# Kernel tuning notes

Measured on AMD Instinct MI355X. Metric: run time of the kernel, lower is better.

The kernel has to match this reference:

```python
import jax, jax.numpy as jnp
import numpy as np

D_EMB = 1024
D_ATTN = 1024
NUM_HEADS = 16
HEAD_DIM = D_ATTN // NUM_HEADS
SEQ = 2048
BS = 2


def setup_inputs() -> dict:
    key = jax.random.key(0)
    ks = jax.random.split(key, 6)
    s = 1.0 / np.sqrt(D_EMB)
    return {
        "x": jax.random.normal(ks[0], (BS, SEQ, D_EMB), dtype=jnp.float32),
        "W_q": jax.random.uniform(ks[1], (D_ATTN, D_EMB), jnp.float32, -s, s),
        "W_k": jax.random.uniform(ks[2], (D_ATTN, D_EMB), jnp.float32, -s, s),
        "W_v": jax.random.uniform(ks[3], (D_ATTN, D_EMB), jnp.float32, -s, s),
        "W_o": jax.random.uniform(ks[4], (D_ATTN, D_ATTN), jnp.float32, -s, s),
        "b_o": jax.random.uniform(ks[5], (D_ATTN,), jnp.float32, -s, s),
    }


def reference(x, W_q, W_k, W_v, W_o, b_o):
    bs, seq_len, _ = x.shape
    # QKV projections (torch Linear: x @ W.T)
    q = jnp.einsum('bse,ae->bsa', x, W_q).reshape(bs, seq_len, NUM_HEADS, HEAD_DIM)
    k = jnp.einsum('bse,ae->bsa', x, W_k).reshape(bs, seq_len, NUM_HEADS, HEAD_DIM)
    v = jnp.einsum('bse,ae->bsa', x, W_v).reshape(bs, seq_len, NUM_HEADS, HEAD_DIM)
    # [b, h, s, d]
    q = q.transpose(0, 2, 1, 3)
    k = k.transpose(0, 2, 1, 3)
    v = v.transpose(0, 2, 1, 3)
    # scores [b, h, s, s] with causal mask
    scores = jnp.einsum('bhqd,bhkd->bhqk', q, k)
    causal = jnp.tril(jnp.ones((seq_len, seq_len), dtype=bool))
    scores = jnp.where(causal, scores, -jnp.inf)
    attn = jax.nn.softmax(scores / np.sqrt(HEAD_DIM), axis=-1)
    # dropout p=0.0 -> identity
    ctx = jnp.einsum('bhqk,bhkd->bhqd', attn, v)
    ctx = ctx.transpose(0, 2, 1, 3).reshape(bs, seq_len, D_ATTN)
    return jnp.einsum('bsa,oa->bso', ctx, W_o) + b_o
```

## Files before the change

### kernel.cpp

```cpp
#include <hip/hip_runtime.h>
#include <stdint.h>

#define SEQ   2048
#define DEMB  1024
#define NH    16
#define HD    64
#define MROWS 4096

typedef __bf16 bf16x8 __attribute__((ext_vector_type(8)));
typedef __bf16 bf16x4 __attribute__((ext_vector_type(4)));
typedef float  f32x4  __attribute__((ext_vector_type(4)));

#define MFMA(a, b, c) __builtin_amdgcn_mfma_f32_16x16x32_bf16((a), (b), (c), 0, 0, 0)
#define VMCNT(n) asm volatile("s_waitcnt vmcnt(" #n ")" ::: "memory")

static __device__ __forceinline__ uint16_t f2bf(float f) {
  union { __bf16 b; uint16_t u; } c;
  c.b = (__bf16)f;
  return c.u;
}

static __device__ __forceinline__ ushort4 pack4(f32x4 f) {
  union { bf16x4 b; ushort4 u; } c;
  c.b[0] = (__bf16)f[0]; c.b[1] = (__bf16)f[1];
  c.b[2] = (__bf16)f[2]; c.b[3] = (__bf16)f[3];
  return c.u;
}

static __device__ __forceinline__ bf16x8 ldb8(const uint16_t* p) {
  union { uint4 i; bf16x8 b; } u;
  u.i = *(const uint4*)p;
  return u.b;
}

static __device__ __forceinline__ void gld_lds16(const uint16_t* g, uint16_t* l) {
  __builtin_amdgcn_global_load_lds(
      (const __attribute__((address_space(1))) uint32_t*)(g),
      (__attribute__((address_space(3))) uint32_t*)(l),
      16, 0, 0);
}

__global__ __launch_bounds__(256) void cvt_all(const float* __restrict__ x,
                                               const float* __restrict__ wq,
                                               const float* __restrict__ wk,
                                               const float* __restrict__ wv,
                                               const float* __restrict__ wo,
                                               uint16_t* __restrict__ xb,
                                               uint16_t* __restrict__ wqkv,
                                               uint16_t* __restrict__ wob) {
  const int bid = blockIdx.x;
  const float* src; uint16_t* dst; int off;
  if (bid < 4096)      { src = x;  dst = xb;                 off = bid; }
  else if (bid < 5120) { src = wq; dst = wqkv;               off = bid - 4096; }
  else if (bid < 6144) { src = wk; dst = wqkv + (1u << 20);  off = bid - 5120; }
  else if (bid < 7168) { src = wv; dst = wqkv + (2u << 20);  off = bid - 6144; }
  else                 { src = wo; dst = wob;                off = bid - 7168; }
  const int i = (off * 256 + threadIdx.x) * 4;
  float4 v = *(const float4*)(src + i);
  f32x4 f; f[0] = v.x; f[1] = v.y; f[2] = v.z; f[3] = v.w;
  *(ushort4*)(dst + i) = pack4(f);
}

__global__ __launch_bounds__(512, 2) void gemm_qkv(const uint16_t* __restrict__ A,
                                                   const uint16_t* __restrict__ B,
                                                   uint16_t* __restrict__ Cq,
                                                   uint16_t* __restrict__ Ck,
                                                   uint16_t* __restrict__ Cvt) {
  constexpr int K = 1024;
  __shared__ uint16_t lds[73728];

  const int bcol = blockIdx.x * 192;
  const int brow = blockIdx.y << 8;

  const int t  = threadIdx.x;
  const int l  = t & 63;
  const int li = l & 15, lg = l >> 4;
  const int w  = t >> 6;
  const int wm = w >> 2;
  const int wn = w & 3;

  const int srow = t >> 3;
  const int scol = ((t & 7) ^ (srow & 7)) << 3;
  const uint16_t* gA = A + (size_t)(brow + srow) * K + scol;
  const uint16_t* gB = B + (size_t)(bcol + srow) * K + scol;

  auto stageA = [&](int buf, int k0) {
    uint16_t* as = lds + buf * 16384;
    gld_lds16(gA + k0,                    as + t * 8);
    gld_lds16(gA + (size_t)64 * K + k0,   as + 4096 + t * 8);
    gld_lds16(gA + (size_t)128 * K + k0,  as + 8192 + t * 8);
    gld_lds16(gA + (size_t)192 * K + k0,  as + 12288 + t * 8);
  };
  auto stageB = [&](int buf, int k0) {
    uint16_t* bs = lds + 49152 + buf * 12288;
    gld_lds16(gB + k0,                    bs + t * 8);
    gld_lds16(gB + (size_t)64 * K + k0,   bs + 4096 + t * 8);
    gld_lds16(gB + (size_t)128 * K + k0,  bs + 8192 + t * 8);
  };

  const int sw = li & 7;
  auto ldA = [&](int buf, int kh, int fi) {
    const int row = wm * 128 + fi * 16 + li;
    return ldb8(&lds[buf * 16384 + (row << 6) + ((((kh << 2) + lg) ^ sw) << 3)]);
  };
  auto ldB = [&](int buf, int kh, int ni) {
    const int row = wn * 48 + ni * 16 + li;
    return ldb8(&lds[49152 + buf * 12288 + (row << 6) + ((((kh << 2) + lg) ^ sw) << 3)]);
  };

  f32x4 acc[8][3] = {};

  stageB(0, 0);
  stageA(0, 0);
  stageA(1, 64);
  VMCNT(4);
  __builtin_amdgcn_s_barrier();

  for (int kt = 0; kt < 16; ++kt) {
    const int k0 = kt << 6;
    if (kt + 1 < 16) stageB((kt + 1) & 1, k0 + 64);
    if (kt + 2 < 16) stageA((kt + 2) % 3, k0 + 128);

    const int ab = kt % 3, bb = kt & 1;
#pragma unroll
    for (int kh = 0; kh < 2; ++kh) {
      bf16x8 af[8], bfr[3];
#pragma unroll
      for (int ni = 0; ni < 3; ++ni) bfr[ni] = ldB(bb, kh, ni);
#pragma unroll
      for (int fi = 0; fi < 8; ++fi) af[fi] = ldA(ab, kh, fi);
      __builtin_amdgcn_s_setprio(1);
#pragma unroll
      for (int fi = 0; fi < 8; ++fi)
#pragma unroll
        for (int ni = 0; ni < 3; ++ni)
          acc[fi][ni] = MFMA(af[fi], bfr[ni], acc[fi][ni]);
      __builtin_amdgcn_s_setprio(0);
    }

    if (kt + 1 < 16) {
      if (kt + 2 < 16) VMCNT(4);
      else             VMCNT(0);
      __builtin_amdgcn_s_barrier();
    }
  }

  __syncthreads();

  uint16_t* slab = lds + w * 6800;
  bool anyV = false;

#pragma unroll
  for (int mi = 0; mi < 8; ++mi) {
#pragma unroll
    for (int ni = 0; ni < 3; ++ni) {
      const int col = bcol + wn * 48 + ni * 16 + li;
      const int row = brow + wm * 128 + mi * 16 + lg * 4;
      if (col < 1024) {
#pragma unroll
        for (int r = 0; r < 4; ++r)
          Cq[(size_t)(row + r) * 1024 + col] = f2bf(acc[mi][ni][r] * 0.18033688f);
      } else if (col < 2048) {
#pragma unroll
        for (int r = 0; r < 4; ++r)
          Ck[(size_t)(row + r) * 1024 + (col - 1024)] = f2bf(acc[mi][ni][r]);
      } else {
        anyV = true;
        *(ushort4*)&slab[(ni * 16 + li) * 136 + mi * 16 + lg * 4] = pack4(acc[mi][ni]);
      }
    }
  }

  if (anyV) {
    asm volatile("s_waitcnt lgkmcnt(0)" ::: "memory");
    const int m0 = brow + wm * 128;
    const size_t mbase = (size_t)((m0 >> 11) << 10) * 2048 + (m0 & 2047);
#pragma unroll
    for (int cc = 0; cc < 12; ++cc) {
      const int c_loc = cc * 4 + lg;
      const int cglob = bcol + wn * 48 + c_loc;
      if (cglob >= 2048) {
        const int c = cglob - 2048;
        uint4 v = *(const uint4*)&slab[c_loc * 136 + li * 8];
        *(uint4*)(Cvt + (size_t)c * 2048 + mbase + li * 8) = v;
      }
    }
  }
}

__global__ __launch_bounds__(512, 2) void gemm_out(const uint16_t* __restrict__ A,
                                                   const uint16_t* __restrict__ B,
                                                   float* __restrict__ Cf,
                                                   const float* __restrict__ bias) {
  constexpr int K = 1024;
  __shared__ uint16_t lds[49152];

  const int bcol = blockIdx.x << 7;
  const int brow = blockIdx.y << 7;

  const int t  = threadIdx.x;
  const int l  = t & 63;
  const int li = l & 15, lg = l >> 4;
  const int w  = t >> 6;
  const int wm = w >> 2;
  const int wn = w & 3;

  const int srow = t >> 3;
  const int scol = ((t & 7) ^ (srow & 7)) << 3;
  const uint16_t* gA = A + (size_t)(brow + srow) * K + scol;
  const uint16_t* gB = B + (size_t)(bcol + srow) * K + scol;

  auto stage = [&](int buf, int k0) {
    uint16_t* as = lds + buf * 8192;
    uint16_t* bs = lds + 24576 + buf * 8192;
    gld_lds16(gA + k0,                  as + t * 8);
    gld_lds16(gA + (size_t)64 * K + k0, as + 4096 + t * 8);
    gld_lds16(gB + k0,                  bs + t * 8);
    gld_lds16(gB + (size_t)64 * K + k0, bs + 4096 + t * 8);
  };

  const int sw = li & 7;
  auto ldA = [&](int buf, int kh, int fi) {
    const int row = wm * 64 + fi * 16 + li;
    return ldb8(&lds[buf * 8192 + (row << 6) + ((((kh << 2) + lg) ^ sw) << 3)]);
  };
  auto ldB = [&](int buf, int kh, int ni) {
    const int row = wn * 32 + ni * 16 + li;
    return ldb8(&lds[24576 + buf * 8192 + (row << 6) + ((((kh << 2) + lg) ^ sw) << 3)]);
  };

  f32x4 acc[4][2] = {};

  stage(0, 0);
  stage(1, 64);
  VMCNT(4);
  __builtin_amdgcn_s_barrier();

  for (int kt = 0; kt < 16; ++kt) {
    const int k0 = kt << 6;
    if (kt + 2 < 16) stage((kt + 2) % 3, k0 + 128);

    const int cb = kt % 3;
#pragma unroll
    for (int kh = 0; kh < 2; ++kh) {
      bf16x8 af[4], bfr[2];
#pragma unroll
      for (int ni = 0; ni < 2; ++ni) bfr[ni] = ldB(cb, kh, ni);
#pragma unroll
      for (int fi = 0; fi < 4; ++fi) af[fi] = ldA(cb, kh, fi);
      __builtin_amdgcn_s_setprio(1);
#pragma unroll
      for (int fi = 0; fi < 4; ++fi)
#pragma unroll
        for (int ni = 0; ni < 2; ++ni)
          acc[fi][ni] = MFMA(af[fi], bfr[ni], acc[fi][ni]);
      __builtin_amdgcn_s_setprio(0);
    }

    if (kt + 1 < 16) {
      if (kt + 2 < 16) VMCNT(4);
      else             VMCNT(0);
      __builtin_amdgcn_s_barrier();
    }
  }

#pragma unroll
  for (int mi = 0; mi < 4; ++mi) {
#pragma unroll
    for (int ni = 0; ni < 2; ++ni) {
      const int row = brow + wm * 64 + mi * 16 + lg * 4;
      const int col = bcol + wn * 32 + ni * 16 + li;
      const float bv = bias[col];
#pragma unroll
      for (int r = 0; r < 4; ++r)
        Cf[(size_t)(row + r) * 1024 + col] = acc[mi][ni][r] + bv;
    }
  }
}

__global__ __launch_bounds__(256, 2) void attn_fwd(const uint16_t* __restrict__ Q,
                                                   const uint16_t* __restrict__ K,
                                                   const uint16_t* __restrict__ Vt,
                                                   uint16_t* __restrict__ ctx) {
  const int id   = blockIdx.x;
  const int rank = id >> 3;
  const int bh   = (id & 7) * 4 + (rank >> 4);
  const int pr   = rank & 15;
  const int b = bh >> 4, h = bh & 15;

  const int t  = threadIdx.x;
  const int w  = t >> 6, l = t & 63;
  const int li = l & 15, lg = l >> 4;

  __shared__ uint16_t Kl[3][64 * 64];
  __shared__ uint16_t Vl[3][64 * 64];
  __shared__ uint16_t P[4][16][72];

  const uint16_t* Kg = K + (size_t)(b * 2048) * 1024 + h * 64;
  const uint16_t* Vg = Vt + (size_t)(b * 1024 + h * 64) * 2048;

  const int srow = t >> 3;
  const int scol = ((t & 7) * 8) ^ ((srow & 7) * 8);

  auto stage = [&](int buf, int kt2) {
    const int kb2 = kt2 << 6;
    gld_lds16(Kg + (size_t)(kb2 + srow) * 1024 + scol,      &Kl[buf][t * 8]);
    gld_lds16(Kg + (size_t)(kb2 + 32 + srow) * 1024 + scol, &Kl[buf][2048 + t * 8]);
    gld_lds16(Vg + (size_t)srow * 2048 + kb2 + scol,        &Vl[buf][t * 8]);
    gld_lds16(Vg + (size_t)(32 + srow) * 2048 + kb2 + scol, &Vl[buf][2048 + t * 8]);
  };

  const int fsw = (li & 7) * 8;

#pragma unroll 1
  for (int ph = 0; ph < 2; ++ph) {
    const int qbl  = ph ? (31 - pr) : pr;
    const int nkt  = qbl + 1;
    const int qrow = (qbl << 6) + (w << 4);
    const uint16_t* qp = Q + (size_t)(b * 2048 + qrow + li) * 1024 + h * 64 + lg * 8;
    const bf16x8 q0 = ldb8(qp);
    const bf16x8 q1 = ldb8(qp + 32);

    f32x4 o[4] = {};
    float l_r = 0.f;

    stage(0, 0);
    stage(1, 1);
    VMCNT(4);
    __builtin_amdgcn_s_barrier();

    for (int kt = 0; kt < nkt; ++kt) {
      if (kt + 2 < nkt) stage((kt + 2) % 3, kt + 2);

      const uint16_t* Kc = &Kl[kt % 3][0];
      const uint16_t* Vc = &Vl[kt % 3][0];

      f32x4 s[4];
      __builtin_amdgcn_s_setprio(1);
#pragma unroll
      for (int tt = 0; tt < 4; ++tt) {
        const uint16_t* kr = Kc + (tt * 16 + li) * 64;
        f32x4 z = {};
        z = MFMA(ldb8(kr + ((lg * 8) ^ fsw)), q0, z);
        z = MFMA(ldb8(kr + ((32 + lg * 8) ^ fsw)), q1, z);
        s[tt] = z;
      }
      __builtin_amdgcn_s_setprio(0);

      bf16x8 vf[4][2];
#pragma unroll
      for (int dt = 0; dt < 4; ++dt) {
        const uint16_t* vr = Vc + (dt * 16 + li) * 64;
        vf[dt][0] = ldb8(vr + ((lg * 8) ^ fsw));
        vf[dt][1] = ldb8(vr + ((32 + lg * 8) ^ fsw));
      }

      if (kt == qbl) {
        const int qloc = (w << 4) + li;
#pragma unroll
        for (int tt = 0; tt < 4; ++tt) {
          const int key = (tt << 4) + (lg << 2);
#pragma unroll
          for (int r = 0; r < 4; ++r)
            if (key + r > qloc) s[tt][r] = -1e30f;
        }
      }

      float lsum = 0.f;
      ushort4 pk[4];
#pragma unroll
      for (int tt = 0; tt < 4; ++tt) {
        f32x4 p;
        p[0] = __builtin_amdgcn_exp2f(s[tt][0]);
        p[1] = __builtin_amdgcn_exp2f(s[tt][1]);
        p[2] = __builtin_amdgcn_exp2f(s[tt][2]);
        p[3] = __builtin_amdgcn_exp2f(s[tt][3]);
        lsum += (p[0] + p[1]) + (p[2] + p[3]);
        pk[tt] = pack4(p);
      }
      l_r += lsum;

#pragma unroll
      for (int tt = 0; tt < 4; ++tt)
        *(ushort4*)&P[w][li][(tt << 4) + (lg << 2)] = pk[tt];
      asm volatile("s_waitcnt lgkmcnt(0)" ::: "memory");

      const bf16x8 pb0 = ldb8(&P[w][li][lg * 8]);
      const bf16x8 pb1 = ldb8(&P[w][li][32 + lg * 8]);
      __builtin_amdgcn_s_setprio(1);
#pragma unroll
      for (int dt = 0; dt < 4; ++dt) {
        o[dt] = MFMA(vf[dt][0], pb0, o[dt]);
        o[dt] = MFMA(vf[dt][1], pb1, o[dt]);
      }
      __builtin_amdgcn_s_setprio(0);

      if (kt + 1 < nkt) {
        if (kt + 2 < nkt) VMCNT(4);
        else              VMCNT(0);
        __builtin_amdgcn_s_barrier();
      }
    }

    __syncthreads();

    l_r += __shfl_xor(l_r, 16);
    l_r += __shfl_xor(l_r, 32);
    const float inv = 1.0f / l_r;
    const int qg = b * 2048 + qrow + li;
#pragma unroll
    for (int dt = 0; dt < 4; ++dt) {
      f32x4 ov = o[dt];
      ov[0] *= inv; ov[1] *= inv; ov[2] *= inv; ov[3] *= inv;
      *(ushort4*)(ctx + (size_t)qg * 1024 + h * 64 + (dt << 4) + (lg << 2)) = pack4(ov);
    }
  }
}

extern "C" void kernel_launch(void* const* d_in, const int* in_sizes, int n_in,
                              void* d_out, int out_size, void* d_ws, size_t ws_size,
                              hipStream_t stream) {
  const float* x  = (const float*)d_in[0];
  const float* Wq = (const float*)d_in[1];
  const float* Wk = (const float*)d_in[2];
  const float* Wv = (const float*)d_in[3];
  const float* Wo = (const float*)d_in[4];
  const float* bo = (const float*)d_in[5];
  float* out = (float*)d_out;

  char* ws = (char*)d_ws;
  uint16_t* xb   = (uint16_t*)(ws);
  uint16_t* Wqkv = (uint16_t*)(ws + ( 8u << 20));
  uint16_t* Wob  = (uint16_t*)(ws + (14u << 20));
  uint16_t* Qb   = (uint16_t*)(ws + (16u << 20));
  uint16_t* Kb   = (uint16_t*)(ws + (24u << 20));
  uint16_t* Vt   = (uint16_t*)(ws + (32u << 20));
  uint16_t* Ctx  = (uint16_t*)(ws);

  cvt_all<<<8192, 256, 0, stream>>>(x, Wq, Wk, Wv, Wo, xb, Wqkv, Wob);

  gemm_qkv<<<dim3(16, 16), 512, 0, stream>>>(xb, Wqkv, Qb, Kb, Vt);

  attn_fwd<<<512, 256, 0, stream>>>(Qb, Kb, Vt, Ctx);

  gemm_out<<<dim3(8, 32), 512, 0, stream>>>(Ctx, Wob, out, bo);
}
```

Before: 100.7 us.

## Interleave GEMM global staging with MFMA sub-phases and pipeline QK^T ahead of PV

The projection GEMM main loop is split into four sub-phases, each a quarter of the k-tile's MFMA work. The next-stage global-to-LDS loads are spread across these sub-phases, with extra barriers keeping waves in lockstep, so memory issue overlaps matrix math instead of being issued in one burst. In the attention kernel, the QK^T scores for the next key tile are computed before the PV MFMAs of the current tile, so the exp/softmax and PV latency can overlap with the next score computation. The risks are the extra barrier overhead and the register cost of the carried scores. The next K tile is also read after only a per-wave vmcnt wait, before the workgroup barrier, which could be a visibility race on LDS data written by other waves.

```diff
diff --git a/kernel.cpp b/kernel.cpp
--- a/kernel.cpp
+++ b/kernel.cpp
@@ -84,18 +84,11 @@
   const uint16_t* gA = A + (size_t)(brow + srow) * K + scol;
   const uint16_t* gB = B + (size_t)(bcol + srow) * K + scol;
 
-  auto stageA = [&](int buf, int k0) {
-    uint16_t* as = lds + buf * 16384;
-    gld_lds16(gA + k0,                    as + t * 8);
-    gld_lds16(gA + (size_t)64 * K + k0,   as + 4096 + t * 8);
-    gld_lds16(gA + (size_t)128 * K + k0,  as + 8192 + t * 8);
-    gld_lds16(gA + (size_t)192 * K + k0,  as + 12288 + t * 8);
-  };
-  auto stageB = [&](int buf, int k0) {
-    uint16_t* bs = lds + 49152 + buf * 12288;
-    gld_lds16(gB + k0,                    bs + t * 8);
-    gld_lds16(gB + (size_t)64 * K + k0,   bs + 4096 + t * 8);
-    gld_lds16(gB + (size_t)128 * K + k0,  bs + 8192 + t * 8);
+  auto stA = [&](int buf, int k0, int i) {
+    gld_lds16(gA + (size_t)(i * 64) * K + k0, lds + buf * 16384 + i * 4096 + t * 8);
+  };
+  auto stB = [&](int buf, int k0, int i) {
+    gld_lds16(gB + (size_t)(i * 64) * K + k0, lds + 49152 + buf * 12288 + i * 4096 + t * 8);
   };
 
   const int sw = li & 7;
@@ -110,39 +103,80 @@
 
   f32x4 acc[8][3] = {};
 
-  stageB(0, 0);
-  stageA(0, 0);
-  stageA(1, 64);
+  stB(0, 0, 0); stB(0, 0, 1); stB(0, 0, 2);
+  stA(0, 0, 0); stA(0, 0, 1); stA(0, 0, 2); stA(0, 0, 3);
+  stA(1, 64, 0); stA(1, 64, 1); stA(1, 64, 2); stA(1, 64, 3);
   VMCNT(4);
   __builtin_amdgcn_s_barrier();
 
   for (int kt = 0; kt < 16; ++kt) {
     const int k0 = kt << 6;
-    if (kt + 1 < 16) stageB((kt + 1) & 1, k0 + 64);
-    if (kt + 2 < 16) stageA((kt + 2) % 3, k0 + 128);
-
     const int ab = kt % 3, bb = kt & 1;
-#pragma unroll
-    for (int kh = 0; kh < 2; ++kh) {
-      bf16x8 af[8], bfr[3];
-#pragma unroll
-      for (int ni = 0; ni < 3; ++ni) bfr[ni] = ldB(bb, kh, ni);
-#pragma unroll
-      for (int fi = 0; fi < 8; ++fi) af[fi] = ldA(ab, kh, fi);
-      __builtin_amdgcn_s_setprio(1);
-#pragma unroll
-      for (int fi = 0; fi < 8; ++fi)
-#pragma unroll
-        for (int ni = 0; ni < 3; ++ni)
-          acc[fi][ni] = MFMA(af[fi], bfr[ni], acc[fi][ni]);
-      __builtin_amdgcn_s_setprio(0);
-    }
+    const int nbA = (kt + 2) % 3, nbB = (kt + 1) & 1;
+    const bool pB = (kt + 1 < 16), pA = (kt + 2 < 16);
+    bf16x8 af[4], b0[3], b1[3];
+
+    if (pB) { stB(nbB, k0 + 64, 0); stB(nbB, k0 + 64, 1); }
+#pragma unroll
+    for (int ni = 0; ni < 3; ++ni) b0[ni] = ldB(bb, 0, ni);
+#pragma unroll
+    for (int fi = 0; fi < 4; ++fi) af[fi] = ldA(ab, 0, fi);
+    __builtin_amdgcn_s_barrier();
+    __builtin_amdgcn_s_setprio(1);
+#pragma unroll
+    for (int fi = 0; fi < 4; ++fi)
+#pragma unroll
+      for (int ni = 0; ni < 3; ++ni)
+        acc[fi][ni] = MFMA(af[fi], b0[ni], acc[fi][ni]);
+    __builtin_amdgcn_s_setprio(0);
+    __builtin_amdgcn_s_barrier();
+
+    if (pB) stB(nbB, k0 + 64, 2);
+    if (pA) stA(nbA, k0 + 128, 0);
+#pragma unroll
+    for (int fi = 0; fi < 4; ++fi) af[fi] = ldA(ab, 0, 4 + fi);
+    __builtin_amdgcn_s_barrier();
+    __builtin_amdgcn_s_setprio(1);
+#pragma unroll
+    for (int fi = 0; fi < 4; ++fi)
+#pragma unroll
+      for (int ni = 0; ni < 3; ++ni)
+        acc[4 + fi][ni] = MFMA(af[fi], b0[ni], acc[4 + fi][ni]);
+    __builtin_amdgcn_s_setprio(0);
+    __builtin_amdgcn_s_barrier();
+
+    if (pA) { stA(nbA, k0 + 128, 1); stA(nbA, k0 + 128, 2); }
+#pragma unroll
+    for (int ni = 0; ni < 3; ++ni) b1[ni] = ldB(bb, 1, ni);
+#pragma unroll
+    for (int fi = 0; fi < 4; ++fi) af[fi] = ldA(ab, 1, fi);
+    __builtin_amdgcn_s_barrier();
+    __builtin_amdgcn_s_setprio(1);
+#pragma unroll
+    for (int fi = 0; fi < 4; ++fi)
+#pragma unroll
+      for (int ni = 0; ni < 3; ++ni)
+        acc[fi][ni] = MFMA(af[fi], b1[ni], acc[fi][ni]);
+    __builtin_amdgcn_s_setprio(0);
+    __builtin_amdgcn_s_barrier();
+
+    if (pA) stA(nbA, k0 + 128, 3);
+#pragma unroll
+    for (int fi = 0; fi < 4; ++fi) af[fi] = ldA(ab, 1, 4 + fi);
+    __builtin_amdgcn_s_barrier();
+    __builtin_amdgcn_s_setprio(1);
+#pragma unroll
+    for (int fi = 0; fi < 4; ++fi)
+#pragma unroll
+      for (int ni = 0; ni < 3; ++ni)
+        acc[4 + fi][ni] = MFMA(af[fi], b1[ni], acc[4 + fi][ni]);
+    __builtin_amdgcn_s_setprio(0);
 
     if (kt + 1 < 16) {
-      if (kt + 2 < 16) VMCNT(4);
-      else             VMCNT(0);
-      __builtin_amdgcn_s_barrier();
-    }
+      if (pA) VMCNT(4);
+      else    VMCNT(0);
+    }
+    __builtin_amdgcn_s_barrier();
   }
 
   __syncthreads();
@@ -329,24 +363,23 @@
     VMCNT(4);
     __builtin_amdgcn_s_barrier();
 
-    for (int kt = 0; kt < nkt; ++kt) {
-      if (kt + 2 < nkt) stage((kt + 2) % 3, kt + 2);
-
-      const uint16_t* Kc = &Kl[kt % 3][0];
-      const uint16_t* Vc = &Vl[kt % 3][0];
-
-      f32x4 s[4];
-      __builtin_amdgcn_s_setprio(1);
+    f32x4 s_cur[4];
+    {
+      const uint16_t* Kc = &Kl[0][0];
 #pragma unroll
       for (int tt = 0; tt < 4; ++tt) {
         const uint16_t* kr = Kc + (tt * 16 + li) * 64;
         f32x4 z = {};
         z = MFMA(ldb8(kr + ((lg * 8) ^ fsw)), q0, z);
         z = MFMA(ldb8(kr + ((32 + lg * 8) ^ fsw)), q1, z);
-        s[tt] = z;
-      }
-      __builtin_amdgcn_s_setprio(0);
-
+        s_cur[tt] = z;
+      }
+    }
+
+    for (int kt = 0; kt < nkt; ++kt) {
+      if (kt + 2 < nkt) stage((kt + 2) % 3, kt + 2);
+
+      const uint16_t* Vc = &Vl[kt % 3][0];
       bf16x8 vf[4][2];
 #pragma unroll
       for (int dt = 0; dt < 4; ++dt) {
@@ -362,7 +395,7 @@
           const int key = (tt << 4) + (lg << 2);
 #pragma unroll
           for (int r = 0; r < 4; ++r)
-            if (key + r > qloc) s[tt][r] = -1e30f;
+            if (key + r > qloc) s_cur[tt][r] = -1e30f;
         }
       }
 
@@ -371,10 +404,10 @@
 #pragma unroll
       for (int tt = 0; tt < 4; ++tt) {
         f32x4 p;
-        p[0] = __builtin_amdgcn_exp2f(s[tt][0]);
-        p[1] = __builtin_amdgcn_exp2f(s[tt][1]);
-        p[2] = __builtin_amdgcn_exp2f(s[tt][2]);
-        p[3] = __builtin_amdgcn_exp2f(s[tt][3]);
+        p[0] = __builtin_amdgcn_exp2f(s_cur[tt][0]);
+        p[1] = __builtin_amdgcn_exp2f(s_cur[tt][1]);
+        p[2] = __builtin_amdgcn_exp2f(s_cur[tt][2]);
+        p[3] = __builtin_amdgcn_exp2f(s_cur[tt][3]);
         lsum += (p[0] + p[1]) + (p[2] + p[3]);
         pk[tt] = pack4(p);
       }
@@ -383,8 +416,25 @@
 #pragma unroll
       for (int tt = 0; tt < 4; ++tt)
         *(ushort4*)&P[w][li][(tt << 4) + (lg << 2)] = pk[tt];
+
+      f32x4 s_nx[4];
+      if (kt + 1 < nkt) {
+        if (kt + 2 < nkt) VMCNT(4);
+        else              VMCNT(0);
+        const uint16_t* Kc = &Kl[(kt + 1) % 3][0];
+        __builtin_amdgcn_s_setprio(1);
+#pragma unroll
+        for (int tt = 0; tt < 4; ++tt) {
+          const uint16_t* kr = Kc + (tt * 16 + li) * 64;
+          f32x4 z = {};
+          z = MFMA(ldb8(kr + ((lg * 8) ^ fsw)), q0, z);
+          z = MFMA(ldb8(kr + ((32 + lg * 8) ^ fsw)), q1, z);
+          s_nx[tt] = z;
+        }
+        __builtin_amdgcn_s_setprio(0);
+      }
+
       asm volatile("s_waitcnt lgkmcnt(0)" ::: "memory");
-
       const bf16x8 pb0 = ldb8(&P[w][li][lg * 8]);
       const bf16x8 pb1 = ldb8(&P[w][li][32 + lg * 8]);
       __builtin_amdgcn_s_setprio(1);
@@ -395,10 +445,11 @@
       }
       __builtin_amdgcn_s_setprio(0);
 
+      __builtin_amdgcn_s_barrier();
+
       if (kt + 1 < nkt) {
-        if (kt + 2 < nkt) VMCNT(4);
-        else              VMCNT(0);
-        __builtin_amdgcn_s_barrier();
+#pragma unroll
+        for (int tt = 0; tt < 4; ++tt) s_cur[tt] = s_nx[tt];
       }
     }
 
```

Measured after the change: 113.7 us. +12.9%, slower.
